# Kernel optimization log

Hardware: AMD Instinct MI355X
Metric: run time of the kernel (lower is better)

The kernel has to match this reference:

```python
import jax, jax.numpy as jnp
import numpy as np

D_MODEL = 1024
N_HEADS = 16
D_K = D_MODEL // N_HEADS
THETA = 10000.0
MAX_SEQ_LEN = 2048


def _rope_tables(seq_len):
    pos = jnp.arange(seq_len, dtype=jnp.float32)
    inv_freq = 1.0 / (THETA ** (jnp.arange(0, D_K, 2, dtype=jnp.float32) / D_K))
    ang = pos[:, None] * inv_freq[None, :]  # [T, D_K/2]
    return jnp.cos(ang), jnp.sin(ang)


def _apply_rope(x, cos, sin):
    # x: [..., T, D_K]; cos/sin: [T, D_K/2]
    x_even = x[..., ::2]
    x_odd = x[..., 1::2]
    r_even = x_even * cos - x_odd * sin
    r_odd = x_even * sin + x_odd * cos
    out = jnp.stack([r_even, r_odd], axis=-1)  # [..., T, D_K/2, 2]
    return out.reshape(x.shape)


def setup_inputs() -> dict:
    key = jax.random.key(0)
    ks = jax.random.split(key, 5)
    std = np.sqrt(2.0 / (D_MODEL + D_MODEL))
    x = jax.random.normal(ks[0], (2, 2048, D_MODEL), dtype=jnp.float32)
    w_q = jax.random.normal(ks[1], (D_MODEL, D_MODEL), dtype=jnp.float32) * std
    w_k = jax.random.normal(ks[2], (D_MODEL, D_MODEL), dtype=jnp.float32) * std
    w_v = jax.random.normal(ks[3], (D_MODEL, D_MODEL), dtype=jnp.float32) * std
    w_o = jax.random.normal(ks[4], (D_MODEL, D_MODEL), dtype=jnp.float32) * std
    return {"x": x, "w_q": w_q, "w_k": w_k, "w_v": w_v, "w_o": w_o}


def reference(x, w_q, w_k, w_v, w_o):
    B, T, _ = x.shape
    # projections: weight stored as [d_out, d_in], y = x @ W^T
    q = jnp.einsum('btd,od->bto', x, w_q)
    k = jnp.einsum('btd,od->bto', x, w_k)
    v = jnp.einsum('btd,od->bto', x, w_v)
    # split heads: [B, T, H*Dk] -> [B, H, T, Dk]
    q = q.reshape(B, T, N_HEADS, D_K).transpose(0, 2, 1, 3)
    k = k.reshape(B, T, N_HEADS, D_K).transpose(0, 2, 1, 3)
    v = v.reshape(B, T, N_HEADS, D_K).transpose(0, 2, 1, 3)
    cos, sin = _rope_tables(T)
    q = _apply_rope(q, cos, sin)
    k = _apply_rope(k, cos, sin)
    scores = jnp.einsum('bhqd,bhkd->bhqk', q, k) / np.sqrt(D_K).astype(np.float32)
    causal = jnp.tril(jnp.ones((T, T), dtype=bool))
    scores = jnp.where(causal, scores, -jnp.inf)
    attn = jax.nn.softmax(scores, axis=-1)
    out = jnp.einsum('bhqk,bhkd->bhqd', attn, v)
    out = out.transpose(0, 2, 1, 3).reshape(B, T, D_MODEL)
    return jnp.einsum('btd,od->bto', out, w_o)
```

## Files before the change

### kernel.cpp

```cpp
#include <hip/hip_runtime.h>
#include <hip/hip_bf16.h>

typedef __bf16 bf16_t;
typedef __bf16 bf16x8 __attribute__((ext_vector_type(8)));
typedef float f32x4 __attribute__((ext_vector_type(4)));
typedef short short4v __attribute__((ext_vector_type(4)));
typedef unsigned int uint2v __attribute__((ext_vector_type(2)));

#define D_MODEL 1024
#define T_SEQ 2048
#define NH 16
#define DKD 64
#define X_ELEMS (4194304u)
#define W_ELEMS (1048576u)
#define Q_SCALE 0.18033688011112042f

__device__ __forceinline__ void async16(const bf16_t* g, bf16_t* l) {
    __builtin_amdgcn_global_load_lds((const __attribute__((address_space(1))) void*)g,
                                     (__attribute__((address_space(3))) void*)l, 16, 0, 0);
}

__global__ __launch_bounds__(256) void convert_kernel(
    const float* __restrict__ x, const float* __restrict__ wq,
    const float* __restrict__ wk, const float* __restrict__ wv,
    const float* __restrict__ wo,
    bf16_t* __restrict__ xb, bf16_t* __restrict__ wqb, bf16_t* __restrict__ wkb,
    bf16_t* __restrict__ wvb, bf16_t* __restrict__ wob)
{
    size_t idx = ((size_t)blockIdx.x * 256 + threadIdx.x) * 4;
    const float* src; bf16_t* dst; size_t off;
    if (idx < X_ELEMS) { src = x; dst = xb; off = idx; }
    else {
        size_t r = idx - X_ELEMS;
        unsigned w = (unsigned)(r >> 20);
        off = r & (W_ELEMS - 1);
        src = (w == 0) ? wq : (w == 1) ? wk : (w == 2) ? wv : wo;
        dst = (w == 0) ? wqb : (w == 1) ? wkb : (w == 2) ? wvb : wob;
    }
    float4 v = *(const float4*)(src + off);
    union { bf16_t b[4]; short4v s; } u;
    u.b[0] = (bf16_t)v.x; u.b[1] = (bf16_t)v.y;
    u.b[2] = (bf16_t)v.z; u.b[3] = (bf16_t)v.w;
    *(short4v*)(dst + off) = u.s;
}

__global__ __launch_bounds__(256) void rope_kernel(float* __restrict__ cost, float* __restrict__ sint)
{
    int idx = blockIdx.x * 256 + threadIdx.x;
    int t = idx >> 5, i = idx & 31;
    float inv = expf(-0.28782313662425572f * (float)i);
    float ang = (float)t * inv;
    float s, c;
    sincosf(ang, &s, &c);
    cost[idx] = c; sint[idx] = s;
}

__global__ __launch_bounds__(256) void gemm_fused(
    const bf16_t* __restrict__ A,
    const bf16_t* __restrict__ W0, const bf16_t* __restrict__ W1, const bf16_t* __restrict__ W2,
    bf16_t* __restrict__ qout, bf16_t* __restrict__ kout, bf16_t* __restrict__ vout,
    const float* __restrict__ cost, const float* __restrict__ sint,
    float* __restrict__ fout, int modeBase)
{
    const int K = 1024;
    __shared__ bf16_t As[128 * 32];
    __shared__ bf16_t Bs[128 * 32];
    const int tid = threadIdx.x;
    const int wave = tid >> 6, lane = tid & 63;
    const int quad = lane >> 4, l16 = lane & 15;
    const int m0 = blockIdx.x * 128;
    const int n0 = blockIdx.y * 128;
    const int wm = (wave >> 1) * 64, wn = (wave & 1) * 64;
    const int mode = modeBase + blockIdx.z;
    const bf16_t* W = (mode == 1) ? W1 : (mode == 2) ? W2 : W0;

    const bf16_t* Afrag = (mode == 2) ? Bs : As;
    const bf16_t* Bfrag = (mode == 2) ? As : Bs;
    const int aoff = (mode == 2) ? wn : wm;
    const int boff = (mode == 2) ? wm : wn;

    const f32x4 fzero = {0.f, 0.f, 0.f, 0.f};
    f32x4 acc[4][4];
    #pragma unroll
    for (int i = 0; i < 4; ++i)
        #pragma unroll
        for (int j = 0; j < 4; ++j) acc[i][j] = fzero;

    for (int k0 = 0; k0 < K; k0 += 32) {
        __syncthreads();
        #pragma unroll
        for (int c = 0; c < 2; ++c) {
            int G = c * 256 + tid;
            int row = G >> 2, go = G & 3;
            async16(A + (size_t)(m0 + row) * K + (k0 + go * 8), As + (size_t)(c * 256 + wave * 64) * 8);
            async16(W + (size_t)(n0 + row) * K + (k0 + go * 8), Bs + (size_t)(c * 256 + wave * 64) * 8);
        }
        __syncthreads();
        bf16x8 af[4], bfv[4];
        #pragma unroll
        for (int mi = 0; mi < 4; ++mi)
            af[mi] = *(const bf16x8*)(Afrag + (aoff + mi * 16 + l16) * 32 + quad * 8);
        #pragma unroll
        for (int ni = 0; ni < 4; ++ni)
            bfv[ni] = *(const bf16x8*)(Bfrag + (boff + ni * 16 + l16) * 32 + quad * 8);
        #pragma unroll
        for (int mi = 0; mi < 4; ++mi)
            #pragma unroll
            for (int ni = 0; ni < 4; ++ni)
                acc[mi][ni] = __builtin_amdgcn_mfma_f32_16x16x32_bf16(af[mi], bfv[ni], acc[mi][ni], 0, 0, 0);
    }

    #pragma unroll
    for (int mi = 0; mi < 4; ++mi) {
        #pragma unroll
        for (int ni = 0; ni < 4; ++ni) {
            #pragma unroll
            for (int reg = 0; reg < 4; ++reg) {
                float v = acc[mi][ni][reg];
                if (mode == 2) {
                    int f   = n0 + wn + mi * 16 + quad * 4 + reg;
                    int tok = m0 + wm + ni * 16 + l16;
                    int t = tok & (T_SEQ - 1), b = tok >> 11;
                    int h = f >> 6, dk = f & 63;
                    vout[(((size_t)b * NH + h) * DKD + dk) * T_SEQ + t] = (bf16_t)v;
                } else {
                    int row = m0 + wm + mi * 16 + quad * 4 + reg;
                    int col = n0 + wn + ni * 16 + l16;
                    if (mode == 3) {
                        fout[(size_t)row * D_MODEL + col] = v;
                    } else {
                        int t = row & (T_SEQ - 1), b = row >> 11;
                        int h = col >> 6, dk = col & 63;
                        float vp = __shfl_xor(v, 1);
                        int fi = dk >> 1;
                        float c = cost[t * 32 + fi], s = sint[t * 32 + fi];
                        float r = (dk & 1) ? (vp * s + v * c) : (v * c - vp * s);
                        if (mode == 0) r *= Q_SCALE;
                        bf16_t* dst = (mode == 0) ? qout : kout;
                        dst[(((size_t)b * NH + h) * T_SEQ + t) * DKD + dk] = (bf16_t)r;
                    }
                }
            }
        }
    }
}

__global__ __launch_bounds__(64, 2) void attn_kernel(
    const bf16_t* __restrict__ Q, const bf16_t* __restrict__ Kb,
    const bf16_t* __restrict__ Vt, bf16_t* __restrict__ O,
    float* __restrict__ Opart, float* __restrict__ Lpart)
{
    const int lane = threadIdx.x;
    const int quad = lane >> 4, l16 = lane & 15;
    const int vq = (((quad & 1) << 1) | (quad >> 1)) * 8;
    const int bh = blockIdx.x;
    const int u = blockIdx.y;
    int y, ktlo, kthi;
    if (u < 32) { y = u + 32; ktlo = 0; kthi = 16; }
    else { y = 95 - u; ktlo = (u < 64) ? 16 : 0; kthi = (y * 32 + 95) >> 6; }
    const int qw = y * 32;

    const bf16_t* kbase = Kb + (size_t)bh * T_SEQ * DKD;
    const bf16_t* vbase = Vt + (size_t)bh * DKD * T_SEQ;

    bf16x8 qf[2][2];
    #pragma unroll
    for (int j = 0; j < 2; ++j) {
        const bf16_t* qp = Q + ((size_t)bh * T_SEQ + qw + j * 16 + l16) * DKD;
        qf[j][0] = *(const bf16x8*)(qp + quad * 8);
        qf[j][1] = *(const bf16x8*)(qp + 32 + quad * 8);
    }
    const f32x4 fzero = {0.f, 0.f, 0.f, 0.f};
    f32x4 oacc[2][4];
    #pragma unroll
    for (int j = 0; j < 2; ++j)
        #pragma unroll
        for (int i = 0; i < 4; ++i) oacc[j][i] = fzero;
    float lsum[2] = {0.f, 0.f};

    bf16x8 ka[4][2], kb2[4][2], vcur[4][2];
    #pragma unroll
    for (int fi = 0; fi < 4; ++fi) {
        const bf16_t* kr = kbase + (size_t)(ktlo * 64 + fi * 16 + l16) * DKD + quad * 8;
        ka[fi][0] = *(const bf16x8*)(kr);
        ka[fi][1] = *(const bf16x8*)(kr + 32);
    }

#define ATT_TILE(KC, KN) do { \
    const int k0 = kt * 64; \
    _Pragma("unroll") \
    for (int di = 0; di < 4; ++di) { \
        const bf16_t* vr = vbase + (size_t)(di * 16 + l16) * T_SEQ + k0 + vq; \
        vcur[di][0] = *(const bf16x8*)(vr); \
        vcur[di][1] = *(const bf16x8*)(vr + 32); \
    } \
    if (kt + 1 < kthi) { \
        _Pragma("unroll") \
        for (int fi = 0; fi < 4; ++fi) { \
            const bf16_t* kr = kbase + (size_t)(k0 + 64 + fi * 16 + l16) * DKD + quad * 8; \
            KN[fi][0] = *(const bf16x8*)(kr); \
            KN[fi][1] = *(const bf16x8*)(kr + 32); \
        } \
    } \
    _Pragma("unroll") \
    for (int j = 0; j < 2; ++j) { \
        if (k0 > qw + j * 16 + 15) continue;    \
        const int qcol = qw + j * 16 + l16; \
        f32x4 s[4]; \
        _Pragma("unroll") \
        for (int fi = 0; fi < 4; ++fi) { \
            f32x4 z = fzero; \
            z = __builtin_amdgcn_mfma_f32_16x16x32_bf16(KC[fi][0], qf[j][0], z, 0, 0, 0); \
            z = __builtin_amdgcn_mfma_f32_16x16x32_bf16(KC[fi][1], qf[j][1], z, 0, 0, 0); \
            s[fi] = z; \
        } \
        if (k0 + 63 > qw + j * 16) { \
            _Pragma("unroll") \
            for (int fi = 0; fi < 4; ++fi) \
                _Pragma("unroll") \
                for (int reg = 0; reg < 4; ++reg) { \
                    int key = k0 + fi * 16 + quad * 4 + reg; \
                    s[fi][reg] = (key > qcol) ? -__builtin_inff() : s[fi][reg]; \
                } \
        } \
        float sm = 0.f; \
        _Pragma("unroll") \
        for (int fi = 0; fi < 4; ++fi) \
            _Pragma("unroll") \
            for (int reg = 0; reg < 4; ++reg) { \
                float p = __builtin_amdgcn_exp2f(s[fi][reg]); \
                s[fi][reg] = p; sm += p; \
            } \
        lsum[j] += sm; \
        unsigned wv[4][2]; \
        _Pragma("unroll") \
        for (int fi = 0; fi < 4; ++fi) { \
            asm("v_cvt_pk_bf16_f32 %0, %1, %2" : "=v"(wv[fi][0]) : "v"(s[fi][0]), "v"(s[fi][1])); \
            asm("v_cvt_pk_bf16_f32 %0, %1, %2" : "=v"(wv[fi][1]) : "v"(s[fi][2]), "v"(s[fi][3])); \
        } \
        uint2v r0 = __builtin_amdgcn_permlane16_swap(wv[0][0], wv[1][0], false, false); \
        uint2v r1 = __builtin_amdgcn_permlane16_swap(wv[0][1], wv[1][1], false, false); \
        uint2v r2 = __builtin_amdgcn_permlane16_swap(wv[2][0], wv[3][0], false, false); \
        uint2v r3 = __builtin_amdgcn_permlane16_swap(wv[2][1], wv[3][1], false, false); \
        union { unsigned uu[4]; bf16x8 v; } p0, p1; \
        p0.uu[0] = r0[0]; p0.uu[1] = r1[0]; p0.uu[2] = r0[1]; p0.uu[3] = r1[1]; \
        p1.uu[0] = r2[0]; p1.uu[1] = r3[0]; p1.uu[2] = r2[1]; p1.uu[3] = r3[1]; \
        _Pragma("unroll") \
        for (int di = 0; di < 4; ++di) { \
            oacc[j][di] = __builtin_amdgcn_mfma_f32_16x16x32_bf16(vcur[di][0], p0.v, oacc[j][di], 0, 0, 0); \
            oacc[j][di] = __builtin_amdgcn_mfma_f32_16x16x32_bf16(vcur[di][1], p1.v, oacc[j][di], 0, 0, 0); \
        } \
    } \
} while (0)

    bool flip = false;
    for (int kt = ktlo; kt < kthi; ++kt) {
        if (!flip) { ATT_TILE(ka, kb2); } else { ATT_TILE(kb2, ka); }
        flip = !flip;
    }
#undef ATT_TILE

    if (u >= 64) {
        const int b = bh >> 4, h = bh & 15;
        #pragma unroll
        for (int j = 0; j < 2; ++j) {
            float l = lsum[j];
            l += __shfl_xor(l, 16);
            l += __shfl_xor(l, 32);
            float rl = 1.0f / l;
            int q = qw + j * 16 + l16;
            #pragma unroll
            for (int di = 0; di < 4; ++di) {
                union { bf16_t hh[4]; unsigned long long u64; } ok;
                #pragma unroll
                for (int reg = 0; reg < 4; ++reg) ok.hh[reg] = (bf16_t)(oacc[j][di][reg] * rl);
                int d = di * 16 + quad * 4;
                *(unsigned long long*)(O + ((size_t)b * T_SEQ + q) * D_MODEL + h * DKD + d) = ok.u64;
            }
        }
    } else {
        const int yy = y - 32;
        const int chunk = (ktlo == 16) ? 1 : 0;
        const size_t slot = ((size_t)bh * 32 + yy) * 2 + chunk;
        float* op = Opart + slot * 2048;
        #pragma unroll
        for (int j = 0; j < 2; ++j) {
            Lpart[slot * 128 + j * 64 + lane] = lsum[j];
            #pragma unroll
            for (int di = 0; di < 4; ++di)
                *(f32x4*)(op + ((size_t)(j * 4 + di) * 64 + lane) * 4) = oacc[j][di];
        }
    }
}

__global__ __launch_bounds__(256) void combine_kernel(
    const float* __restrict__ Opart, const float* __restrict__ Lpart, bf16_t* __restrict__ O)
{
    const int bh = blockIdx.x, yy = blockIdx.y;
    const int t = threadIdx.x;
    const int ql = t >> 3;
    const int d0 = (t & 7) * 8;
    const int j = ql >> 4, l16 = ql & 15;
    const size_t a = (size_t)bh * 32 + yy;
    const float* A0 = Opart + a * 2 * 2048;
    const float* A1 = A0 + 2048;
    const float* L = Lpart + a * 2 * 128 + j * 64 + l16;
    float l = 0.f;
    #pragma unroll
    for (int q = 0; q < 4; ++q) l += L[q * 16] + L[128 + q * 16];
    const float rl = 1.0f / l;
    const int di = d0 >> 4;
    const int quad0 = (d0 & 15) >> 2;
    union { bf16_t h[8]; bf16x8 v; } ov;
    #pragma unroll
    for (int g = 0; g < 2; ++g) {
        const int off = ((j * 4 + di) * 64 + (quad0 + g) * 16 + l16) * 4;
        f32x4 x0 = *(const f32x4*)(A0 + off);
        f32x4 x1 = *(const f32x4*)(A1 + off);
        #pragma unroll
        for (int reg = 0; reg < 4; ++reg)
            ov.h[g * 4 + reg] = (bf16_t)((x0[reg] + x1[reg]) * rl);
    }
    const int b = bh >> 4, h = bh & 15;
    const int q = 1024 + yy * 32 + ql;
    *(bf16x8*)(O + ((size_t)b * T_SEQ + q) * D_MODEL + h * DKD + d0) = ov.v;
}

extern "C" void kernel_launch(void* const* d_in, const int* in_sizes, int n_in,
                              void* d_out, int out_size, void* d_ws, size_t ws_size,
                              hipStream_t stream)
{
    const float* x  = (const float*)d_in[0];
    const float* wq = (const float*)d_in[1];
    const float* wk = (const float*)d_in[2];
    const float* wv = (const float*)d_in[3];
    const float* wo = (const float*)d_in[4];
    float* out = (float*)d_out;

    char* ws = (char*)d_ws;
    size_t off = 0;
    auto alloc = [&](size_t bytes) -> void* {
        void* p = ws + off; off += (bytes + 255) & ~(size_t)255; return p;
    };
    bf16_t* xb   = (bf16_t*)alloc((size_t)X_ELEMS * 2);
    bf16_t* wqb  = (bf16_t*)alloc((size_t)W_ELEMS * 2);
    bf16_t* wkb  = (bf16_t*)alloc((size_t)W_ELEMS * 2);
    bf16_t* wvb  = (bf16_t*)alloc((size_t)W_ELEMS * 2);
    bf16_t* wob  = (bf16_t*)alloc((size_t)W_ELEMS * 2);
    bf16_t* qb   = (bf16_t*)alloc((size_t)X_ELEMS * 2);
    bf16_t* kb   = (bf16_t*)alloc((size_t)X_ELEMS * 2);
    bf16_t* vtb  = (bf16_t*)alloc((size_t)X_ELEMS * 2);
    bf16_t* ob   = (bf16_t*)alloc((size_t)X_ELEMS * 2);
    float*  cost = (float*)alloc((size_t)T_SEQ * 32 * 4);
    float*  sint = (float*)alloc((size_t)T_SEQ * 32 * 4);
    float*  opart = (float*)alloc((size_t)2048 * 2048 * 4);
    float*  lpart = (float*)alloc((size_t)2048 * 128 * 4);

    convert_kernel<<<8192, 256, 0, stream>>>(x, wq, wk, wv, wo, xb, wqb, wkb, wvb, wob);
    rope_kernel<<<256, 256, 0, stream>>>(cost, sint);
    gemm_fused<<<dim3(32, 8, 3), 256, 0, stream>>>(xb, wqb, wkb, wvb, qb, kb, vtb, cost, sint, nullptr, 0);
    attn_kernel<<<dim3(32, 96), 64, 0, stream>>>(qb, kb, vtb, ob, opart, lpart);
    combine_kernel<<<dim3(32, 32), 256, 0, stream>>>(opart, lpart, ob);
    gemm_fused<<<dim3(32, 8, 1), 256, 0, stream>>>(ob, wob, nullptr, nullptr, nullptr, nullptr, nullptr,
                                                   cost, sint, out, 3);
}
```

Before: 222.4 us.

## Double-buffer V tiles in LDS via async global-to-LDS prefetch in attention

The attention kernel no longer loads the V fragments straight from global memory at the start of each key tile. It now prefetches the next 64-key V tile into a double-buffered, XOR-swizzled LDS array with global_load_lds, and reads the current tile back with inline-asm ds_read_b128 before the PV MFMAs. The aim is to hide V global-load latency behind the current tile's compute and cut register pressure from the vcur array. In exchange it adds 16KB of LDS per block, which can limit occupancy. It also depends on the vmcnt waits the compiler inserts for the K loads to cover completion of the async LDS writes, since the inline asm only waits on lgkmcnt.

```diff
diff --git a/kernel.cpp b/kernel.cpp
--- a/kernel.cpp
+++ b/kernel.cpp
@@ -18,6 +18,10 @@
 __device__ __forceinline__ void async16(const bf16_t* g, bf16_t* l) {
     __builtin_amdgcn_global_load_lds((const __attribute__((address_space(1))) void*)g,
                                      (__attribute__((address_space(3))) void*)l, 16, 0, 0);
+}
+
+__device__ __forceinline__ unsigned ldsa(const bf16_t* p) {
+    return (unsigned)(size_t)(const __attribute__((address_space(3))) bf16_t*)p;
 }
 
 __global__ __launch_bounds__(256) void convert_kernel(
@@ -150,9 +154,11 @@
     const bf16_t* __restrict__ Vt, bf16_t* __restrict__ O,
     float* __restrict__ Opart, float* __restrict__ Lpart)
 {
+    __shared__ bf16_t Vs[2][4096];
     const int lane = threadIdx.x;
     const int quad = lane >> 4, l16 = lane & 15;
-    const int vq = (((quad & 1) << 1) | (quad >> 1)) * 8;
+    const int sig = ((quad & 1) << 1) | (quad >> 1);
+    const int m7 = l16 & 7;
     const int bh = blockIdx.x;
     const int u = blockIdx.y;
     int y, ktlo, kthi;
@@ -163,6 +169,14 @@
     const bf16_t* kbase = Kb + (size_t)bh * T_SEQ * DKD;
     const bf16_t* vbase = Vt + (size_t)bh * DKD * T_SEQ;
 
+    const int vrow = lane >> 3;
+    const bf16_t* vsrc = vbase + (size_t)vrow * T_SEQ + (((lane & 7) ^ vrow) * 8);
+
+    const unsigned o0 = (unsigned)((l16 * 64 + ((sig ^ m7) * 8)) << 1);
+    const unsigned o1 = (unsigned)((l16 * 64 + (((sig + 4) ^ m7) * 8)) << 1);
+    const unsigned vbase0 = ldsa(Vs[0]);
+    const unsigned vbase1 = ldsa(Vs[1]);
+
     bf16x8 qf[2][2];
     #pragma unroll
     for (int j = 0; j < 2; ++j) {
@@ -178,7 +192,12 @@
         for (int i = 0; i < 4; ++i) oacc[j][i] = fzero;
     float lsum[2] = {0.f, 0.f};
 
-    bf16x8 ka[4][2], kb2[4][2], vcur[4][2];
+    #pragma unroll
+    for (int c = 0; c < 8; ++c)
+        async16(vsrc + (ktlo * 64) + c * 16384, &Vs[0][0] + c * 512);
+    __builtin_amdgcn_sched_barrier(0);
+
+    bf16x8 ka[4][2], kb2[4][2];
     #pragma unroll
     for (int fi = 0; fi < 4; ++fi) {
         const bf16_t* kr = kbase + (size_t)(ktlo * 64 + fi * 16 + l16) * DKD + quad * 8;
@@ -186,14 +205,14 @@
         ka[fi][1] = *(const bf16x8*)(kr + 32);
     }
 
-#define ATT_TILE(KC, KN) do { \
+#define ATT_TILE(KC, KN, VRB, VST) do { \
     const int k0 = kt * 64; \
-    _Pragma("unroll") \
-    for (int di = 0; di < 4; ++di) { \
-        const bf16_t* vr = vbase + (size_t)(di * 16 + l16) * T_SEQ + k0 + vq; \
-        vcur[di][0] = *(const bf16x8*)(vr); \
-        vcur[di][1] = *(const bf16x8*)(vr + 32); \
+    if (kt + 1 < kthi) { \
+        _Pragma("unroll") \
+        for (int c = 0; c < 8; ++c) \
+            async16(vsrc + (k0 + 64) + c * 16384, (VST) + c * 512); \
     } \
+    __builtin_amdgcn_sched_barrier(0); \
     if (kt + 1 < kthi) { \
         _Pragma("unroll") \
         for (int fi = 0; fi < 4; ++fi) { \
@@ -245,17 +264,39 @@
         union { unsigned uu[4]; bf16x8 v; } p0, p1; \
         p0.uu[0] = r0[0]; p0.uu[1] = r1[0]; p0.uu[2] = r0[1]; p0.uu[3] = r1[1]; \
         p1.uu[0] = r2[0]; p1.uu[1] = r3[0]; p1.uu[2] = r2[1]; p1.uu[3] = r3[1]; \
-        _Pragma("unroll") \
-        for (int di = 0; di < 4; ++di) { \
-            oacc[j][di] = __builtin_amdgcn_mfma_f32_16x16x32_bf16(vcur[di][0], p0.v, oacc[j][di], 0, 0, 0); \
-            oacc[j][di] = __builtin_amdgcn_mfma_f32_16x16x32_bf16(vcur[di][1], p1.v, oacc[j][di], 0, 0, 0); \
-        } \
+         \
+        const unsigned aA = (VRB) + o0, aB = (VRB) + o1; \
+        bf16x8 w0a, w0b, w1a, w1b, w2a, w2b, w3a, w3b; \
+        __builtin_amdgcn_sched_barrier(0); \
+        asm volatile( \
+            "ds_read_b128 %0, %8 offset:0\n\t" \
+            "ds_read_b128 %1, %9 offset:0\n\t" \
+            "ds_read_b128 %2, %8 offset:2048\n\t" \
+            "ds_read_b128 %3, %9 offset:2048\n\t" \
+            "ds_read_b128 %4, %8 offset:4096\n\t" \
+            "ds_read_b128 %5, %9 offset:4096\n\t" \
+            "ds_read_b128 %6, %8 offset:6144\n\t" \
+            "ds_read_b128 %7, %9 offset:6144\n\t" \
+            "s_waitcnt lgkmcnt(0)" \
+            : "=&v"(w0a), "=&v"(w0b), "=&v"(w1a), "=&v"(w1b), \
+              "=&v"(w2a), "=&v"(w2b), "=&v"(w3a), "=&v"(w3b) \
+            : "v"(aA), "v"(aB)); \
+        __builtin_amdgcn_sched_barrier(0); \
+        oacc[j][0] = __builtin_amdgcn_mfma_f32_16x16x32_bf16(w0a, p0.v, oacc[j][0], 0, 0, 0); \
+        oacc[j][0] = __builtin_amdgcn_mfma_f32_16x16x32_bf16(w0b, p1.v, oacc[j][0], 0, 0, 0); \
+        oacc[j][1] = __builtin_amdgcn_mfma_f32_16x16x32_bf16(w1a, p0.v, oacc[j][1], 0, 0, 0); \
+        oacc[j][1] = __builtin_amdgcn_mfma_f32_16x16x32_bf16(w1b, p1.v, oacc[j][1], 0, 0, 0); \
+        oacc[j][2] = __builtin_amdgcn_mfma_f32_16x16x32_bf16(w2a, p0.v, oacc[j][2], 0, 0, 0); \
+        oacc[j][2] = __builtin_amdgcn_mfma_f32_16x16x32_bf16(w2b, p1.v, oacc[j][2], 0, 0, 0); \
+        oacc[j][3] = __builtin_amdgcn_mfma_f32_16x16x32_bf16(w3a, p0.v, oacc[j][3], 0, 0, 0); \
+        oacc[j][3] = __builtin_amdgcn_mfma_f32_16x16x32_bf16(w3b, p1.v, oacc[j][3], 0, 0, 0); \
     } \
 } while (0)
 
     bool flip = false;
     for (int kt = ktlo; kt < kthi; ++kt) {
-        if (!flip) { ATT_TILE(ka, kb2); } else { ATT_TILE(kb2, ka); }
+        if (!flip) { ATT_TILE(ka, kb2, vbase0, &Vs[1][0]); }
+        else       { ATT_TILE(kb2, ka, vbase1, &Vs[0][0]); }
         flip = !flip;
     }
 #undef ATT_TILE
```

Result: faster. 199.7 us (-10.2%).

## Share K/V tiles across four waves via double-buffered LDS in attention

Applied to the files above, without the earlier changes.

The attention kernel moves from one-wave blocks with K/V read straight from global memory to four-wave blocks. Each block streams a 64-key K/V tile into double-buffered, XOR-swizzled shared memory with async global-to-LDS loads, and each wave reads it with ds_read_b128. Work is repartitioned into 128-query groups split into key chunks of up to eight tiles, so the partial-output layout and the combine kernel change to sum a variable number of chunks. The goal is to cut redundant global K/V traffic by reusing each tile across waves. In exchange it adds block-wide barriers on every tile and waits that drain all LDS reads.

```diff
diff --git a/kernel.cpp b/kernel.cpp
--- a/kernel.cpp
+++ b/kernel.cpp
@@ -18,6 +18,10 @@
 __device__ __forceinline__ void async16(const bf16_t* g, bf16_t* l) {
     __builtin_amdgcn_global_load_lds((const __attribute__((address_space(1))) void*)g,
                                      (__attribute__((address_space(3))) void*)l, 16, 0, 0);
+}
+
+__device__ __forceinline__ unsigned ldsa(const bf16_t* p) {
+    return (unsigned)(size_t)(const __attribute__((address_space(3))) bf16_t*)p;
 }
 
 __global__ __launch_bounds__(256) void convert_kernel(
@@ -145,23 +149,48 @@
     }
 }
 
-__global__ __launch_bounds__(64, 2) void attn_kernel(
+__global__ __launch_bounds__(256, 4) void attn_kernel(
     const bf16_t* __restrict__ Q, const bf16_t* __restrict__ Kb,
     const bf16_t* __restrict__ Vt, bf16_t* __restrict__ O,
     float* __restrict__ Opart, float* __restrict__ Lpart)
 {
-    const int lane = threadIdx.x;
+    __shared__ bf16_t Vs[2][4096];
+    __shared__ bf16_t Ks[2][4096];
+    const int tid = threadIdx.x;
+    const int w = tid >> 6;
+    const int lane = tid & 63;
     const int quad = lane >> 4, l16 = lane & 15;
-    const int vq = (((quad & 1) << 1) | (quad >> 1)) * 8;
+    const int sig = ((quad & 1) << 1) | (quad >> 1);
+    const int m7 = l16 & 15 & 7;
     const int bh = blockIdx.x;
-    const int u = blockIdx.y;
-    int y, ktlo, kthi;
-    if (u < 32) { y = u + 32; ktlo = 0; kthi = 16; }
-    else { y = 95 - u; ktlo = (u < 64) ? 16 : 0; kthi = (y * 32 + 95) >> 6; }
-    const int qw = y * 32;
+
+    int v = 39 - (int)blockIdx.y;
+    int g = 0, po = 0;
+    for (;; ++g) {
+        const int C = (g + 4) >> 2;
+        if (v < C) break;
+        v -= C;
+        if (g >= 4) po += C;
+    }
+    const int c = v;
+    const int ktlo = 8 * c;
+    const int kthi = min(8 * c + 8, 2 * g + 2);
+    const int qw = (4 * g + w) * 32;
 
     const bf16_t* kbase = Kb + (size_t)bh * T_SEQ * DKD;
     const bf16_t* vbase = Vt + (size_t)bh * DKD * T_SEQ;
+
+    const int srow = tid >> 3;
+    const int sgr  = (tid & 7) ^ (srow & 7);
+    const bf16_t* vsrc = vbase + (size_t)srow * T_SEQ + sgr * 8;
+    const bf16_t* ksrc = kbase + (size_t)srow * DKD + sgr * 8;
+
+    const unsigned o0  = (unsigned)((l16 * 64 + ((sig ^ m7) * 8)) << 1);
+    const unsigned o1  = (unsigned)((l16 * 64 + (((sig + 4) ^ m7) * 8)) << 1);
+    const unsigned ko0 = (unsigned)((l16 * 64 + ((quad ^ m7) * 8)) << 1);
+    const unsigned ko1 = (unsigned)((l16 * 64 + (((quad + 4) ^ m7) * 8)) << 1);
+    const unsigned vb0 = ldsa(Vs[0]), vb1 = ldsa(Vs[1]);
+    const unsigned kb0 = ldsa(Ks[0]), kb1 = ldsa(Ks[1]);
 
     bf16x8 qf[2][2];
     #pragma unroll
@@ -178,42 +207,57 @@
         for (int i = 0; i < 4; ++i) oacc[j][i] = fzero;
     float lsum[2] = {0.f, 0.f};
 
-    bf16x8 ka[4][2], kb2[4][2], vcur[4][2];
-    #pragma unroll
-    for (int fi = 0; fi < 4; ++fi) {
-        const bf16_t* kr = kbase + (size_t)(ktlo * 64 + fi * 16 + l16) * DKD + quad * 8;
-        ka[fi][0] = *(const bf16x8*)(kr);
-        ka[fi][1] = *(const bf16x8*)(kr + 32);
-    }
-
-#define ATT_TILE(KC, KN) do { \
+    {
+        const bf16_t* vs_ = vsrc + ktlo * 64;
+        const bf16_t* ks_ = ksrc + (size_t)ktlo * 64 * DKD;
+        async16(vs_,         &Vs[0][0] + w * 512);
+        async16(vs_ + 65536, &Vs[0][0] + 2048 + w * 512);
+        async16(ks_,         &Ks[0][0] + w * 512);
+        async16(ks_ + 2048,  &Ks[0][0] + 2048 + w * 512);
+    }
+    asm volatile("s_waitcnt vmcnt(0)" ::: "memory");
+    __syncthreads();
+
+#define ATT_TILE(VNP, KNP, VCA, KCA) do { \
     const int k0 = kt * 64; \
-    _Pragma("unroll") \
-    for (int di = 0; di < 4; ++di) { \
-        const bf16_t* vr = vbase + (size_t)(di * 16 + l16) * T_SEQ + k0 + vq; \
-        vcur[di][0] = *(const bf16x8*)(vr); \
-        vcur[di][1] = *(const bf16x8*)(vr + 32); \
+    if (kt + 1 < kthi) { \
+        const bf16_t* vs_ = vsrc + (k0 + 64); \
+        const bf16_t* ks_ = ksrc + (size_t)(k0 + 64) * DKD; \
+        async16(vs_,         (VNP) + w * 512); \
+        async16(vs_ + 65536, (VNP) + 2048 + w * 512); \
+        async16(ks_,         (KNP) + w * 512); \
+        async16(ks_ + 2048,  (KNP) + 2048 + w * 512); \
     } \
-    if (kt + 1 < kthi) { \
-        _Pragma("unroll") \
-        for (int fi = 0; fi < 4; ++fi) { \
-            const bf16_t* kr = kbase + (size_t)(k0 + 64 + fi * 16 + l16) * DKD + quad * 8; \
-            KN[fi][0] = *(const bf16x8*)(kr); \
-            KN[fi][1] = *(const bf16x8*)(kr + 32); \
-        } \
-    } \
+    __builtin_amdgcn_sched_barrier(0); \
+    bf16x8 kc00, kc01, kc10, kc11, kc20, kc21, kc30, kc31; \
+    { const unsigned kaA = (KCA) + ko0, kaB = (KCA) + ko1; \
+      asm volatile( \
+        "ds_read_b128 %0, %8 offset:0\n\t" \
+        "ds_read_b128 %1, %9 offset:0\n\t" \
+        "ds_read_b128 %2, %8 offset:2048\n\t" \
+        "ds_read_b128 %3, %9 offset:2048\n\t" \
+        "ds_read_b128 %4, %8 offset:4096\n\t" \
+        "ds_read_b128 %5, %9 offset:4096\n\t" \
+        "ds_read_b128 %6, %8 offset:6144\n\t" \
+        "ds_read_b128 %7, %9 offset:6144\n\t" \
+        "s_waitcnt lgkmcnt(0)" \
+        : "=&v"(kc00), "=&v"(kc01), "=&v"(kc10), "=&v"(kc11), \
+          "=&v"(kc20), "=&v"(kc21), "=&v"(kc30), "=&v"(kc31) \
+        : "v"(kaA), "v"(kaB)); } \
+    __builtin_amdgcn_sched_barrier(0); \
     _Pragma("unroll") \
     for (int j = 0; j < 2; ++j) { \
-        if (k0 > qw + j * 16 + 15) continue;    \
+      if (k0 <= qw + j * 16 + 15) {    \
         const int qcol = qw + j * 16 + l16; \
         f32x4 s[4]; \
-        _Pragma("unroll") \
-        for (int fi = 0; fi < 4; ++fi) { \
-            f32x4 z = fzero; \
-            z = __builtin_amdgcn_mfma_f32_16x16x32_bf16(KC[fi][0], qf[j][0], z, 0, 0, 0); \
-            z = __builtin_amdgcn_mfma_f32_16x16x32_bf16(KC[fi][1], qf[j][1], z, 0, 0, 0); \
-            s[fi] = z; \
-        } \
+        s[0] = __builtin_amdgcn_mfma_f32_16x16x32_bf16(kc00, qf[j][0], fzero, 0, 0, 0); \
+        s[0] = __builtin_amdgcn_mfma_f32_16x16x32_bf16(kc01, qf[j][1], s[0], 0, 0, 0); \
+        s[1] = __builtin_amdgcn_mfma_f32_16x16x32_bf16(kc10, qf[j][0], fzero, 0, 0, 0); \
+        s[1] = __builtin_amdgcn_mfma_f32_16x16x32_bf16(kc11, qf[j][1], s[1], 0, 0, 0); \
+        s[2] = __builtin_amdgcn_mfma_f32_16x16x32_bf16(kc20, qf[j][0], fzero, 0, 0, 0); \
+        s[2] = __builtin_amdgcn_mfma_f32_16x16x32_bf16(kc21, qf[j][1], s[2], 0, 0, 0); \
+        s[3] = __builtin_amdgcn_mfma_f32_16x16x32_bf16(kc30, qf[j][0], fzero, 0, 0, 0); \
+        s[3] = __builtin_amdgcn_mfma_f32_16x16x32_bf16(kc31, qf[j][1], s[3], 0, 0, 0); \
         if (k0 + 63 > qw + j * 16) { \
             _Pragma("unroll") \
             for (int fi = 0; fi < 4; ++fi) \
@@ -242,25 +286,54 @@
         uint2v r1 = __builtin_amdgcn_permlane16_swap(wv[0][1], wv[1][1], false, false); \
         uint2v r2 = __builtin_amdgcn_permlane16_swap(wv[2][0], wv[3][0], false, false); \
         uint2v r3 = __builtin_amdgcn_permlane16_swap(wv[2][1], wv[3][1], false, false); \
-        union { unsigned uu[4]; bf16x8 v; } p0, p1; \
+        union { unsigned uu[4]; bf16x8 vv; } p0, p1; \
         p0.uu[0] = r0[0]; p0.uu[1] = r1[0]; p0.uu[2] = r0[1]; p0.uu[3] = r1[1]; \
         p1.uu[0] = r2[0]; p1.uu[1] = r3[0]; p1.uu[2] = r2[1]; p1.uu[3] = r3[1]; \
-        _Pragma("unroll") \
-        for (int di = 0; di < 4; ++di) { \
-            oacc[j][di] = __builtin_amdgcn_mfma_f32_16x16x32_bf16(vcur[di][0], p0.v, oacc[j][di], 0, 0, 0); \
-            oacc[j][di] = __builtin_amdgcn_mfma_f32_16x16x32_bf16(vcur[di][1], p1.v, oacc[j][di], 0, 0, 0); \
-        } \
+        const unsigned vA = (VCA) + o0, vB = (VCA) + o1; \
+        bf16x8 w0a, w0b, w1a, w1b; \
+        __builtin_amdgcn_sched_barrier(0); \
+        asm volatile( \
+            "ds_read_b128 %0, %4 offset:0\n\t" \
+            "ds_read_b128 %1, %5 offset:0\n\t" \
+            "ds_read_b128 %2, %4 offset:2048\n\t" \
+            "ds_read_b128 %3, %5 offset:2048\n\t" \
+            "s_waitcnt lgkmcnt(0)" \
+            : "=&v"(w0a), "=&v"(w0b), "=&v"(w1a), "=&v"(w1b) \
+            : "v"(vA), "v"(vB)); \
+        __builtin_amdgcn_sched_barrier(0); \
+        oacc[j][0] = __builtin_amdgcn_mfma_f32_16x16x32_bf16(w0a, p0.vv, oacc[j][0], 0, 0, 0); \
+        oacc[j][0] = __builtin_amdgcn_mfma_f32_16x16x32_bf16(w0b, p1.vv, oacc[j][0], 0, 0, 0); \
+        oacc[j][1] = __builtin_amdgcn_mfma_f32_16x16x32_bf16(w1a, p0.vv, oacc[j][1], 0, 0, 0); \
+        oacc[j][1] = __builtin_amdgcn_mfma_f32_16x16x32_bf16(w1b, p1.vv, oacc[j][1], 0, 0, 0); \
+        bf16x8 w2a, w2b, w3a, w3b; \
+        asm volatile( \
+            "ds_read_b128 %0, %4 offset:4096\n\t" \
+            "ds_read_b128 %1, %5 offset:4096\n\t" \
+            "ds_read_b128 %2, %4 offset:6144\n\t" \
+            "ds_read_b128 %3, %5 offset:6144\n\t" \
+            "s_waitcnt lgkmcnt(0)" \
+            : "=&v"(w2a), "=&v"(w2b), "=&v"(w3a), "=&v"(w3b) \
+            : "v"(vA), "v"(vB)); \
+        __builtin_amdgcn_sched_barrier(0); \
+        oacc[j][2] = __builtin_amdgcn_mfma_f32_16x16x32_bf16(w2a, p0.vv, oacc[j][2], 0, 0, 0); \
+        oacc[j][2] = __builtin_amdgcn_mfma_f32_16x16x32_bf16(w2b, p1.vv, oacc[j][2], 0, 0, 0); \
+        oacc[j][3] = __builtin_amdgcn_mfma_f32_16x16x32_bf16(w3a, p0.vv, oacc[j][3], 0, 0, 0); \
+        oacc[j][3] = __builtin_amdgcn_mfma_f32_16x16x32_bf16(w3b, p1.vv, oacc[j][3], 0, 0, 0); \
+      } \
     } \
+    asm volatile("s_waitcnt vmcnt(0)" ::: "memory"); \
+    __syncthreads(); \
 } while (0)
 
     bool flip = false;
     for (int kt = ktlo; kt < kthi; ++kt) {
-        if (!flip) { ATT_TILE(ka, kb2); } else { ATT_TILE(kb2, ka); }
+        if (!flip) { ATT_TILE(&Vs[1][0], &Ks[1][0], vb0, kb0); }
+        else       { ATT_TILE(&Vs[0][0], &Ks[0][0], vb1, kb1); }
         flip = !flip;
     }
 #undef ATT_TILE
 
-    if (u >= 64) {
+    if (g < 4) {
         const int b = bh >> 4, h = bh & 15;
         #pragma unroll
         for (int j = 0; j < 2; ++j) {
@@ -279,13 +352,11 @@
             }
         }
     } else {
-        const int yy = y - 32;
-        const int chunk = (ktlo == 16) ? 1 : 0;
-        const size_t slot = ((size_t)bh * 32 + yy) * 2 + chunk;
-        float* op = Opart + slot * 2048;
+        const size_t slot = (size_t)bh * 36 + po + c;
+        float* op = Opart + slot * 8192 + (size_t)w * 2048;
         #pragma unroll
         for (int j = 0; j < 2; ++j) {
-            Lpart[slot * 128 + j * 64 + lane] = lsum[j];
+            Lpart[slot * 512 + w * 128 + j * 64 + lane] = lsum[j];
             #pragma unroll
             for (int di = 0; di < 4; ++di)
                 *(f32x4*)(op + ((size_t)(j * 4 + di) * 64 + lane) * 4) = oacc[j][di];
@@ -296,34 +367,42 @@
 __global__ __launch_bounds__(256) void combine_kernel(
     const float* __restrict__ Opart, const float* __restrict__ Lpart, bf16_t* __restrict__ O)
 {
-    const int bh = blockIdx.x, yy = blockIdx.y;
+    const int bh = blockIdx.x;
+    const int g = 4 + blockIdx.y;
+    const int C = (g + 4) >> 2;
+    int po0 = 0;
+    for (int gg = 4; gg < g; ++gg) po0 += (gg + 4) >> 2;
     const int t = threadIdx.x;
     const int ql = t >> 3;
     const int d0 = (t & 7) * 8;
     const int j = ql >> 4, l16 = ql & 15;
-    const size_t a = (size_t)bh * 32 + yy;
-    const float* A0 = Opart + a * 2 * 2048;
-    const float* A1 = A0 + 2048;
-    const float* L = Lpart + a * 2 * 128 + j * 64 + l16;
-    float l = 0.f;
-    #pragma unroll
-    for (int q = 0; q < 4; ++q) l += L[q * 16] + L[128 + q * 16];
-    const float rl = 1.0f / l;
     const int di = d0 >> 4;
     const int quad0 = (d0 & 15) >> 2;
-    union { bf16_t h[8]; bf16x8 v; } ov;
-    #pragma unroll
-    for (int g = 0; g < 2; ++g) {
-        const int off = ((j * 4 + di) * 64 + (quad0 + g) * 16 + l16) * 4;
-        f32x4 x0 = *(const f32x4*)(A0 + off);
-        f32x4 x1 = *(const f32x4*)(A1 + off);
-        #pragma unroll
-        for (int reg = 0; reg < 4; ++reg)
-            ov.h[g * 4 + reg] = (bf16_t)((x0[reg] + x1[reg]) * rl);
-    }
     const int b = bh >> 4, h = bh & 15;
-    const int q = 1024 + yy * 32 + ql;
-    *(bf16x8*)(O + ((size_t)b * T_SEQ + q) * D_MODEL + h * DKD + d0) = ov.v;
+    const size_t sb = (size_t)bh * 36 + po0;
+
+    for (int w = 0; w < 4; ++w) {
+        float l = 0.f;
+        for (int cc = 0; cc < C; ++cc) {
+            const float* L = Lpart + (sb + cc) * 512 + w * 128 + j * 64 + l16;
+            #pragma unroll
+            for (int q = 0; q < 4; ++q) l += L[q * 16];
+        }
+        const float rl = 1.0f / l;
+        union { bf16_t hh[8]; bf16x8 vv; } ov;
+        #pragma unroll
+        for (int g2 = 0; g2 < 2; ++g2) {
+            const int off = ((j * 4 + di) * 64 + (quad0 + g2) * 16 + l16) * 4;
+            f32x4 acc = {0.f, 0.f, 0.f, 0.f};
+            for (int cc = 0; cc < C; ++cc)
+                acc += *(const f32x4*)(Opart + (sb + cc) * 8192 + (size_t)w * 2048 + off);
+            #pragma unroll
+            for (int reg = 0; reg < 4; ++reg)
+                ov.hh[g2 * 4 + reg] = (bf16_t)(acc[reg] * rl);
+        }
+        const int q = g * 128 + w * 32 + ql;
+        *(bf16x8*)(O + ((size_t)b * T_SEQ + q) * D_MODEL + h * DKD + d0) = ov.vv;
+    }
 }
 
 extern "C" void kernel_launch(void* const* d_in, const int* in_sizes, int n_in,
@@ -353,14 +432,14 @@
     bf16_t* ob   = (bf16_t*)alloc((size_t)X_ELEMS * 2);
     float*  cost = (float*)alloc((size_t)T_SEQ * 32 * 4);
     float*  sint = (float*)alloc((size_t)T_SEQ * 32 * 4);
-    float*  opart = (float*)alloc((size_t)2048 * 2048 * 4);
-    float*  lpart = (float*)alloc((size_t)2048 * 128 * 4);
+    float*  opart = (float*)alloc((size_t)32 * 36 * 8192 * 4);
+    float*  lpart = (float*)alloc((size_t)32 * 36 * 512 * 4);
 
     convert_kernel<<<8192, 256, 0, stream>>>(x, wq, wk, wv, wo, xb, wqb, wkb, wvb, wob);
     rope_kernel<<<256, 256, 0, stream>>>(cost, sint);
     gemm_fused<<<dim3(32, 8, 3), 256, 0, stream>>>(xb, wqb, wkb, wvb, qb, kb, vtb, cost, sint, nullptr, 0);
-    attn_kernel<<<dim3(32, 96), 64, 0, stream>>>(qb, kb, vtb, ob, opart, lpart);
-    combine_kernel<<<dim3(32, 32), 256, 0, stream>>>(opart, lpart, ob);
+    attn_kernel<<<dim3(32, 40), 256, 0, stream>>>(qb, kb, vtb, ob, opart, lpart);
+    combine_kernel<<<dim3(32, 12), 256, 0, stream>>>(opart, lpart, ob);
     gemm_fused<<<dim3(32, 8, 1), 256, 0, stream>>>(ob, wob, nullptr, nullptr, nullptr, nullptr, nullptr,
                                                    cost, sint, out, 3);
 }
```

Measured after the change: 202.6 us. 8.9% less time.
